# Kernel tuning notes

Measured on AMD Instinct MI355X. Metric: run time of the kernel, lower is better.

Reference implementation:

```python
import jax, jax.numpy as jnp
import numpy as np

# dims
T, B, D = 128, 512, 512          # seq, batch, d_input = dim_aug_state*n_agent
M, H, DH, DFF = 6, 2, 32, 64     # mem_len, heads, d_head_inner, d_ff_inner
ACT = 64                          # dim_action*n_agent
BG = 0.1                          # GRU-gate bias (GTrXL)


def _ln(t, g, b):
    mu = t.mean(-1, keepdims=True)
    var = ((t - mu) ** 2).mean(-1, keepdims=True)
    return (t - mu) / jnp.sqrt(var + 1e-5) * g + b


def _rel_shift(x):
    # x: [T, J, B, H] -> TransformerXL relative shift
    Tq, J = x.shape[0], x.shape[1]
    zp = jnp.zeros((Tq, 1) + x.shape[2:], x.dtype)
    x = jnp.concatenate([zp, x], axis=1)              # [T, J+1, B, H]
    x = x.reshape((J + 1, Tq) + x.shape[2:])[1:]      # [J, T, B, H]
    return x.reshape((Tq, J) + x.shape[2:])


def _gate(x, y, W, b):
    # GRU-style gating g(x, y): x = residual stream, y = new branch output
    lin = lambda t, i: t @ W[i] + b[i]
    r = jax.nn.sigmoid(lin(y, 0) + lin(x, 1))
    z = jax.nn.sigmoid(lin(y, 2) + lin(x, 3) - BG)
    h = jnp.tanh(lin(y, 4) + (r * x) @ W[5] + b[5])
    return (1.0 - z) * x + z * h


def setup_inputs() -> dict:
    key = jax.random.key(0)
    ks = iter(jax.random.split(key, 32))
    rn = lambda shape, s=0.02: jax.random.normal(next(ks), shape, jnp.float32) * s
    return dict(
        aug_states=jax.random.normal(next(ks), (T, B, D), jnp.float32),
        action=jax.random.normal(next(ks), (B, ACT), jnp.float32),
        memory=jnp.zeros((M, B, D), jnp.float32),
        W_q=rn((D, H * DH)), W_kv=rn((D, 2 * H * DH)), W_p=rn((D, H * DH)), W_out=rn((H * DH, D)),
        u=rn((H, DH)), v=rn((H, DH)),
        ln1_g=jnp.ones(D), ln1_b=jnp.zeros(D), ln2_g=jnp.ones(D), ln2_b=jnp.zeros(D),
        ff_W1=rn((D, DFF)), ff_b1=jnp.zeros(DFF), ff_W2=rn((DFF, D)), ff_b2=jnp.zeros(D),
        g1_W=rn((6, D, D)), g1_b=jnp.zeros((6, D)), g2_W=rn((6, D, D)), g2_b=jnp.zeros((6, D)),
        d1_W=rn((D, 1024)), d1_b=jnp.zeros(1024),
        d2_W=rn((1024 + ACT, 512)), d2_b=jnp.zeros(512),
        d3_W=rn((512, 300)), d3_b=jnp.zeros(300),
        d4_W=rn((300, 1)), d4_b=jnp.zeros(1),
    )


def reference(aug_states, action, memory, W_q, W_kv, W_p, W_out, u, v,
              ln1_g, ln1_b, ln2_g, ln2_b, ff_W1, ff_b1, ff_W2, ff_b2,
              g1_W, g1_b, g2_W, g2_b, d1_W, d1_b, d2_W, d2_b, d3_W, d3_b, d4_W, d4_b):
    x = aug_states                                    # [T, B, D]
    J = T + M
    # sinusoidal relative position embeddings for positions J-1 .. 0
    pos = jnp.arange(J - 1, -1, -1.0, dtype=jnp.float32)
    inv_freq = 1.0 / (10000.0 ** (jnp.arange(0, D, 2, dtype=jnp.float32) / D))
    si = pos[:, None] * inv_freq[None, :]
    pos_emb = jnp.concatenate([jnp.sin(si), jnp.cos(si)], axis=-1)   # [J, D]

    # --- stable (pre-LN + gated) TransformerXL layer ---
    src2 = _ln(x, ln1_g, ln1_b)
    cat = jnp.concatenate([memory, src2], axis=0)     # [J, B, D]
    k, vv = jnp.split(cat @ W_kv, 2, axis=-1)
    q = (src2 @ W_q).reshape(T, B, H, DH)
    k = k.reshape(J, B, H, DH)
    vv = vv.reshape(J, B, H, DH)
    p = (pos_emb @ W_p).reshape(J, H, DH)
    content = jnp.einsum("ibhd,jbhd->ijbh", q + u, k)
    position = _rel_shift(jnp.einsum("ibhd,jhd->ijbh", q + v, p))
    attn = content + position                         # [T, J, B, H]
    mask = jnp.arange(J)[None, :] > (jnp.arange(T)[:, None] + M)     # causal w/ memory offset
    attn = jnp.where(mask[:, :, None, None], -jnp.inf, attn)
    attn = jax.nn.softmax(attn * (1.0 / np.sqrt(DH)), axis=1)
    av = jnp.einsum("ijbh,jbhd->ibhd", attn, vv).reshape(T, B, H * DH)
    src = _gate(x, av @ W_out, g1_W, g1_b)
    ff = jax.nn.relu(_ln(src, ln2_g, ln2_b) @ ff_W1 + ff_b1) @ ff_W2 + ff_b2
    out = _gate(src, ff, g2_W, g2_b)                  # [T, B, D]

    # --- mean pool + MLP critic head ---
    ts = out.mean(axis=0)                             # [B, D]
    h1 = jax.nn.relu(ts @ d1_W + d1_b)
    h = jnp.concatenate([h1, action], axis=1)
    h = jax.nn.relu(h @ d2_W + d2_b)
    h = jax.nn.relu(h @ d3_W + d3_b)
    return jax.nn.relu(h @ d4_W + d4_b)               # [B, 1]
```

## Files before the change

### kernel.cpp

```cpp
#include <hip/hip_runtime.h>
#include <math.h>

namespace {

constexpr int kT = 128, kB = 512, kD = 512, kM = 6, kH = 2;
constexpr int kJ = kT + kM;
constexpr float kBG = 0.1f;
constexpr int kTB = kT * kB;
constexpr int kBK = 32;

typedef __attribute__((ext_vector_type(8))) short bf16x8;
typedef __attribute__((ext_vector_type(4))) float f32x4;
typedef __attribute__((ext_vector_type(8))) unsigned short us8;
typedef __attribute__((ext_vector_type(4))) unsigned short us4;

__device__ __forceinline__ float sigmoidf_(float x) {
  return 1.0f / (1.0f + __expf(-x));
}

__device__ __forceinline__ unsigned short bf16u(float f) {
  union { float f; unsigned u; } c; c.f = f;
  unsigned r = c.u + 0x7fffu + ((c.u >> 16) & 1u);
  return (unsigned short)(r >> 16);
}

__device__ __forceinline__ float b2f(unsigned short u) {
  union { unsigned u; float f; } c; c.u = (unsigned)u << 16;
  return c.f;
}

__device__ __forceinline__ void gl_lds16(const void* g, void* l) {
  __builtin_amdgcn_global_load_lds(
      (const __attribute__((address_space(1))) unsigned int*)g,
      (__attribute__((address_space(3))) unsigned int*)l, 16, 0, 0);
}

__global__ __launch_bounds__(256) void transp_kernel(const float* __restrict__ W,
                                                     unsigned short* __restrict__ Wt,
                                                     int K, int N) {
  __shared__ float t[32][33];
  const int n0 = blockIdx.x * 32, k0 = blockIdx.y * 32;
  const float* Wb = W + (size_t)blockIdx.z * K * N;
  unsigned short* Wtb = Wt + (size_t)blockIdx.z * K * N;
  int tx = threadIdx.x & 31, ty = threadIdx.x >> 5;
#pragma unroll
  for (int r = 0; r < 32; r += 8)
    t[ty + r][tx] = Wb[(size_t)(k0 + ty + r) * N + n0 + tx];
  __syncthreads();
#pragma unroll
  for (int r = 0; r < 32; r += 8)
    Wtb[(size_t)(n0 + ty + r) * K + k0 + tx] = bf16u(t[tx][ty + r]);
}

__global__ __launch_bounds__(256) void conv_bf16_kernel(const float* __restrict__ in,
                                                        unsigned short* __restrict__ outb,
                                                        size_t n) {
  size_t idx = ((size_t)blockIdx.x * 256 + threadIdx.x) * 8;
  if (idx >= n) return;
  float4 a = *(const float4*)(in + idx);
  float4 c = *(const float4*)(in + idx + 4);
  us8 o;
  o[0] = bf16u(a.x); o[1] = bf16u(a.y); o[2] = bf16u(a.z); o[3] = bf16u(a.w);
  o[4] = bf16u(c.x); o[5] = bf16u(c.y); o[6] = bf16u(c.z); o[7] = bf16u(c.w);
  *(us8*)(outb + idx) = o;
}

__global__ __launch_bounds__(256) void ln1_dual_kernel(const float* __restrict__ in,
                                                       const float* __restrict__ g,
                                                       const float* __restrict__ b,
                                                       unsigned short* __restrict__ outLN,
                                                       unsigned short* __restrict__ outRaw,
                                                       int nrows) {
  int wave = threadIdx.x >> 6, lane = threadIdx.x & 63;
  int row = blockIdx.x * 4 + wave;
  if (row >= nrows) return;
  const float* p = in + (size_t)row * kD + lane * 8;
  float4 a = *(const float4*)p;
  float4 c = *(const float4*)(p + 4);
  float v[8] = {a.x, a.y, a.z, a.w, c.x, c.y, c.z, c.w};
  float s = 0.f;
#pragma unroll
  for (int i = 0; i < 8; ++i) s += v[i];
#pragma unroll
  for (int off = 32; off; off >>= 1) s += __shfl_xor(s, off);
  float mu = s * (1.0f / 512.0f);
  float q = 0.f;
#pragma unroll
  for (int i = 0; i < 8; ++i) { float d = v[i] - mu; q += d * d; }
#pragma unroll
  for (int off = 32; off; off >>= 1) q += __shfl_xor(q, off);
  float rstd = rsqrtf(q * (1.0f / 512.0f) + 1e-5f);
  us8 oln, oraw;
#pragma unroll
  for (int i = 0; i < 8; ++i) {
    int col = lane * 8 + i;
    oln[i] = bf16u((v[i] - mu) * rstd * g[col] + b[col]);
    oraw[i] = bf16u(v[i]);
  }
  size_t off8 = (size_t)row * kD + lane * 8;
  *(us8*)(outLN + off8) = oln;
  *(us8*)(outRaw + off8) = oraw;
}

__global__ __launch_bounds__(256) void ln_b16_kernel(const unsigned short* __restrict__ in,
                                                     const float* __restrict__ g,
                                                     const float* __restrict__ b,
                                                     unsigned short* __restrict__ outb,
                                                     int nrows) {
  int wave = threadIdx.x >> 6, lane = threadIdx.x & 63;
  int row = blockIdx.x * 4 + wave;
  if (row >= nrows) return;
  us8 iv = *(const us8*)(in + (size_t)row * kD + lane * 8);
  float v[8];
#pragma unroll
  for (int i = 0; i < 8; ++i) v[i] = b2f(iv[i]);
  float s = 0.f;
#pragma unroll
  for (int i = 0; i < 8; ++i) s += v[i];
#pragma unroll
  for (int off = 32; off; off >>= 1) s += __shfl_xor(s, off);
  float mu = s * (1.0f / 512.0f);
  float q = 0.f;
#pragma unroll
  for (int i = 0; i < 8; ++i) { float d = v[i] - mu; q += d * d; }
#pragma unroll
  for (int off = 32; off; off >>= 1) q += __shfl_xor(q, off);
  float rstd = rsqrtf(q * (1.0f / 512.0f) + 1e-5f);
  us8 o;
#pragma unroll
  for (int i = 0; i < 8; ++i) {
    int col = lane * 8 + i;
    o[i] = bf16u((v[i] - mu) * rstd * g[col] + b[col]);
  }
  *(us8*)(outb + (size_t)row * kD + lane * 8) = o;
}

template <int TN, int EPI>
__global__ __launch_bounds__(256) void mfma_gemm_bt(
    const unsigned short* __restrict__ A, const unsigned short* __restrict__ Bt,
    int K, const float* __restrict__ bias, void* __restrict__ Cv, int N) {
  constexpr int MI = (TN == 128) ? 4 : 2;
  constexpr int NJ = 4;
  constexpr int BCH = TN * 64 / 1024;
  __shared__ __align__(16) unsigned short As[2][128 * kBK];
  __shared__ __align__(16) unsigned short Bs[2][TN * kBK];
  const int tid = threadIdx.x;
  const int lane = tid & 63, wv = tid >> 6;
  const int ml = lane & 15, qd = lane >> 4;
  const int m0 = blockIdx.y * 128, n0 = blockIdx.x * TN;
  const int mw0 = (TN == 128) ? (wv >> 1) * 64 : wv * 32;
  const int nw0 = (TN == 128) ? (wv & 1) * 64 : 0;
  const size_t ldA = (size_t)K * 2, ldB = (size_t)K * 2;
  const char* Ab = (const char*)A + (size_t)m0 * ldA;
  const char* Bb = (const char*)Bt + (size_t)n0 * ldB;
  auto stg = [&](int k0, int buf) {
#pragma unroll
    for (int c = wv; c < 8; c += 4) {
      int fb = c * 1024 + lane * 16;
      gl_lds16(Ab + (size_t)(fb >> 6) * ldA + (fb & 63) + (size_t)k0 * 2,
               (char*)As[buf] + c * 1024);
    }
#pragma unroll
    for (int c = wv; c < BCH; c += 4) {
      int fb = c * 1024 + lane * 16;
      gl_lds16(Bb + (size_t)(fb >> 6) * ldB + (fb & 63) + (size_t)k0 * 2,
               (char*)Bs[buf] + c * 1024);
    }
  };
  f32x4 acc[MI][NJ];
#pragma unroll
  for (int i = 0; i < MI; ++i)
#pragma unroll
    for (int j = 0; j < NJ; ++j) acc[i][j] = (f32x4)0.f;
  stg(0, 0);
  __syncthreads();
  int cur = 0;
  for (int k0 = 0; k0 < K; k0 += kBK) {
    if (k0 + kBK < K) stg(k0 + kBK, cur ^ 1);
    bf16x8 af[MI], bfr[NJ];
#pragma unroll
    for (int i = 0; i < MI; ++i)
      af[i] = *(const bf16x8*)(As[cur] + (mw0 + i * 16 + ml) * kBK + qd * 8);
#pragma unroll
    for (int j = 0; j < NJ; ++j)
      bfr[j] = *(const bf16x8*)(Bs[cur] + (nw0 + j * 16 + ml) * kBK + qd * 8);
#pragma unroll
    for (int i = 0; i < MI; ++i)
#pragma unroll
      for (int j = 0; j < NJ; ++j)
        acc[i][j] = __builtin_amdgcn_mfma_f32_16x16x32_bf16(af[i], bfr[j], acc[i][j], 0, 0, 0);
    __syncthreads();
    cur ^= 1;
  }
#pragma unroll
  for (int i = 0; i < MI; ++i)
#pragma unroll
    for (int j = 0; j < NJ; ++j)
#pragma unroll
      for (int r = 0; r < 4; ++r) {
        int m = m0 + mw0 + i * 16 + qd * 4 + r;
        int n = n0 + nw0 + j * 16 + ml;
        float val = acc[i][j][r];
        if (EPI >= 2) val += bias[n];
        if (EPI == 2) val = fmaxf(val, 0.f);
        size_t idx = (size_t)m * N + n;
        if (EPI == 0) ((float*)Cv)[idx] = val;
        else ((unsigned short*)Cv)[idx] = bf16u(val);
      }
}

template <int NBLOG>
__device__ __forceinline__ void xcd_decode(int& m0, int& n0, int tileN) {
  const int L = blockIdx.x;
  const int xcd = L & 7;
  const int s = L >> 3;
  const int mgPerX = (int)(gridDim.x >> (3 + NBLOG));
  const int mg = xcd * mgPerX + (s >> NBLOG);
  const int nb = s & ((1 << NBLOG) - 1);
  m0 = mg * 128;
  n0 = nb * tileN;
}

__global__ __launch_bounds__(512, 4) void mfma_gate_r(
    const unsigned short* __restrict__ Yb, const unsigned short* __restrict__ Xb,
    const unsigned short* __restrict__ Wt, const float* __restrict__ gb,
    unsigned short* __restrict__ RX) {
  __shared__ __align__(16) unsigned short As[2][128 * kBK];
  __shared__ __align__(16) unsigned short Bs[2][256 * kBK];
  const int tid = threadIdx.x;
  const int lane = tid & 63, wv = tid >> 6;
  const int ml = lane & 15, qd = lane >> 4;
  int m0, n0;
  xcd_decode<1>(m0, n0, 256);
  const int mw0 = (wv & 1) * 64, nw0 = (wv >> 1) * 64;
  const size_t ld = (size_t)kD * 2;
  const size_t DD = (size_t)kD * kD;
  const char* Abp[2], *Bbp[2];
  {
    const unsigned short* Ap[2] = {Yb, Xb};
#pragma unroll
    for (int p = 0; p < 2; ++p) {
      Abp[p] = (const char*)Ap[p] + (size_t)m0 * ld;
      Bbp[p] = (const char*)(Wt + (size_t)p * DD) + (size_t)n0 * ld;
    }
  }
  auto stg = [&](const char* Ab, const char* Bb, int k0, int buf) {
    {
      int fb = wv * 1024 + lane * 16;
      gl_lds16(Ab + (size_t)(fb >> 6) * ld + (fb & 63) + (size_t)k0 * 2,
               (char*)As[buf] + wv * 1024);
    }
#pragma unroll
    for (int c = wv; c < 16; c += 8) {
      int fb = c * 1024 + lane * 16;
      gl_lds16(Bb + (size_t)(fb >> 6) * ld + (fb & 63) + (size_t)k0 * 2,
               (char*)Bs[buf] + c * 1024);
    }
  };
  f32x4 acc[4][4];
#pragma unroll
  for (int i = 0; i < 4; ++i)
#pragma unroll
    for (int j = 0; j < 4; ++j) acc[i][j] = (f32x4)0.f;
  stg(Abp[0], Bbp[0], 0, 0);
  __syncthreads();
  int cur = 0;
#pragma unroll
  for (int p = 0; p < 2; ++p) {
    for (int k = 0; k < 16; ++k) {
      if (k < 15) stg(Abp[p], Bbp[p], (k + 1) * kBK, cur ^ 1);
      else if (p < 1) stg(Abp[p + 1], Bbp[p + 1], 0, cur ^ 1);
      bf16x8 af[4], bfr[4];
#pragma unroll
      for (int i = 0; i < 4; ++i)
        af[i] = *(const bf16x8*)(As[cur] + (mw0 + i * 16 + ml) * kBK + qd * 8);
#pragma unroll
      for (int j = 0; j < 4; ++j)
        bfr[j] = *(const bf16x8*)(Bs[cur] + (nw0 + j * 16 + ml) * kBK + qd * 8);
#pragma unroll
      for (int i = 0; i < 4; ++i)
#pragma unroll
        for (int j = 0; j < 4; ++j)
          acc[i][j] = __builtin_amdgcn_mfma_f32_16x16x32_bf16(af[i], bfr[j], acc[i][j], 0, 0, 0);
      __syncthreads();
      cur ^= 1;
    }
  }
#pragma unroll
  for (int i = 0; i < 4; ++i)
#pragma unroll
    for (int j = 0; j < 4; ++j)
#pragma unroll
      for (int r = 0; r < 4; ++r) {
        int m = m0 + mw0 + i * 16 + qd * 4 + r;
        int n = n0 + nw0 + j * 16 + ml;
        float rg = sigmoidf_(acc[i][j][r] + gb[n] + gb[kD + n]);
        size_t idx = (size_t)m * kD + n;
        RX[idx] = bf16u(rg * b2f(Xb[idx]));
      }
}

template <bool POOL>
__global__ __launch_bounds__(512, 4) void mfma_gate_hz(
    const unsigned short* __restrict__ Yb, const unsigned short* __restrict__ RXb,
    const unsigned short* __restrict__ Xb, const unsigned short* __restrict__ Wt,
    const float* __restrict__ gb, unsigned short* __restrict__ OUTb,
    float* __restrict__ TS, int rowoff) {
  __shared__ __align__(16) unsigned short As[2][128 * kBK];
  __shared__ __align__(16) unsigned short Bs[2][128 * kBK];
  const int tid = threadIdx.x;
  const int lane = tid & 63, wv = tid >> 6;
  const int ml = lane & 15, qd = lane >> 4;
  int m0, n0;
  xcd_decode<2>(m0, n0, 128);
  const int mw0 = (wv & 3) * 32, nw0 = (wv >> 2) * 64;
  const size_t ld = (size_t)kD * 2;
  const size_t DD = (size_t)kD * kD;
  f32x4 accH[2][4], accZ[2][4];
#pragma unroll
  for (int i = 0; i < 2; ++i)
#pragma unroll
    for (int j = 0; j < 4; ++j) { accH[i][j] = (f32x4)0.f; accZ[i][j] = (f32x4)0.f; }
  const char* Abp[4], *Bbp[4];
  {
    const unsigned short* Ap[4] = {Yb, RXb, Yb, Xb};
    const int wsel[4] = {4, 5, 2, 3};
#pragma unroll
    for (int p = 0; p < 4; ++p) {
      Abp[p] = (const char*)Ap[p] + (size_t)m0 * ld;
      Bbp[p] = (const char*)(Wt + (size_t)wsel[p] * DD) + (size_t)n0 * ld;
    }
  }
  auto stg = [&](const char* Ab, const char* Bb, int k0, int buf) {
    int fb = wv * 1024 + lane * 16;
    size_t go = (size_t)(fb >> 6) * ld + (fb & 63) + (size_t)k0 * 2;
    gl_lds16(Ab + go, (char*)As[buf] + wv * 1024);
    gl_lds16(Bb + go, (char*)Bs[buf] + wv * 1024);
  };
  stg(Abp[0], Bbp[0], 0, 0);
  __syncthreads();
  int cur = 0;
#pragma unroll
  for (int p = 0; p < 4; ++p) {
    f32x4 (*acc)[4] = (p < 2) ? accH : accZ;
    for (int k = 0; k < 16; ++k) {
      if (k < 15) stg(Abp[p], Bbp[p], (k + 1) * kBK, cur ^ 1);
      else if (p < 3) stg(Abp[p + 1], Bbp[p + 1], 0, cur ^ 1);
      bf16x8 af[2], bfr[4];
#pragma unroll
      for (int i = 0; i < 2; ++i)
        af[i] = *(const bf16x8*)(As[cur] + (mw0 + i * 16 + ml) * kBK + qd * 8);
#pragma unroll
      for (int j = 0; j < 4; ++j)
        bfr[j] = *(const bf16x8*)(Bs[cur] + (nw0 + j * 16 + ml) * kBK + qd * 8);
#pragma unroll
      for (int i = 0; i < 2; ++i)
#pragma unroll
        for (int j = 0; j < 4; ++j)
          acc[i][j] = __builtin_amdgcn_mfma_f32_16x16x32_bf16(af[i], bfr[j], acc[i][j], 0, 0, 0);
      __syncthreads();
      cur ^= 1;
    }
  }
#pragma unroll
  for (int i = 0; i < 2; ++i)
#pragma unroll
    for (int j = 0; j < 4; ++j)
#pragma unroll
      for (int r = 0; r < 4; ++r) {
        int m = m0 + mw0 + i * 16 + qd * 4 + r;
        int n = n0 + nw0 + j * 16 + ml;
        float z = sigmoidf_(accZ[i][j][r] + gb[2 * kD + n] + gb[3 * kD + n] - kBG);
        float hc = tanhf(accH[i][j][r] + gb[4 * kD + n] + gb[5 * kD + n]);
        size_t idx = (size_t)m * kD + n;
        float val = (1.0f - z) * b2f(Xb[idx]) + z * hc;
        if (POOL) {
          int b = (rowoff + m) & (kB - 1);
          atomicAdd(TS + (size_t)b * kD + n, val * (1.0f / kT));
        } else {
          OUTb[idx] = bf16u(val);
        }
      }
}

__global__ __launch_bounds__(64) void posp_kernel(const float* __restrict__ Wp,
                                                  float* __restrict__ P) {
  __shared__ float emb[512];
  int jj = blockIdx.x;
  int t = threadIdx.x;
  float pos = (float)(kJ - 1 - jj);
#pragma unroll
  for (int r = 0; r < 8; ++r) {
    int d = t + r * 64;
    int i = (d < 256) ? d : d - 256;
    float invf = expf(-((float)(2 * i) * (1.0f / 512.0f)) * 9.210340371976184f);
    float si = pos * invf;
    emb[d] = (d < 256) ? sinf(si) : cosf(si);
  }
  __syncthreads();
  float acc = 0.f;
  for (int d = 0; d < 512; ++d) acc = fmaf(emb[d], Wp[d * 64 + t], acc);
  P[jj * 64 + t] = acc;
}

__global__ __launch_bounds__(128) void attn_kernel(
    const float* __restrict__ Q, const unsigned short* __restrict__ KV,
    const float* __restrict__ P, const float* __restrict__ U,
    const float* __restrict__ V, unsigned short* __restrict__ AV) {
  __shared__ float ks[kJ][32];
  __shared__ float vs[kJ][32];
  __shared__ float ps[32][kJ + 2];
  const int b = blockIdx.x, h = blockIdx.y;
  const int tid = threadIdx.x;
  for (int idx = tid; idx < kJ * 8; idx += 128) {
    int j = idx >> 3, seg = idx & 7;
    const unsigned short* src = KV + ((size_t)(j * kB + b)) * 128 + h * 32 + seg * 4;
    us4 kq = *(const us4*)src;
    us4 vq = *(const us4*)(src + 64);
#pragma unroll
    for (int e = 0; e < 4; ++e) {
      ks[j][seg * 4 + e] = b2f(kq[e]);
      vs[j][seg * 4 + e] = b2f(vq[e]);
    }
  }
  for (int idx = tid; idx < kJ * 8; idx += 128) {
    int j = idx >> 3, seg = idx & 7;
    float4 pq = *(const float4*)(P + j * 64 + h * 32 + seg * 4);
    ps[seg * 4 + 0][j] = pq.x;
    ps[seg * 4 + 1][j] = pq.y;
    ps[seg * 4 + 2][j] = pq.z;
    ps[seg * 4 + 3][j] = pq.w;
  }
  __syncthreads();
  const int i = tid;
  float qu[32], qv[32];
  const float* qp = Q + ((size_t)(i * kB + b)) * 64 + h * 32;
#pragma unroll
  for (int d = 0; d < 32; ++d) {
    float qd = qp[d];
    qu[d] = qd + U[h * 32 + d];
    qv[d] = qd + V[h * 32 + d];
  }
  float m = -INFINITY, l = 0.f, acc[32] = {};
  const float scale = 0.17677669529663687f;
  for (int j = 0; j <= i + kM; ++j) {
    float s = 0.f;
#pragma unroll
    for (int d = 0; d < 32; d += 4) {
      float4 k4 = *(const float4*)&ks[j][d];
      s = fmaf(qu[d + 0], k4.x, s);
      s = fmaf(qu[d + 1], k4.y, s);
      s = fmaf(qu[d + 2], k4.z, s);
      s = fmaf(qu[d + 3], k4.w, s);
    }
    int jj = j + (kT - 1) - i;
#pragma unroll
    for (int d = 0; d < 32; ++d) s = fmaf(qv[d], ps[d][jj], s);
    float ls = s * scale;
    float nm = fmaxf(m, ls);
    float w = __expf(ls - nm);
    float f = __expf(m - nm);
    l = l * f + w;
#pragma unroll
    for (int d = 0; d < 32; d += 4) {
      float4 v4 = *(const float4*)&vs[j][d];
      acc[d + 0] = fmaf(acc[d + 0], f, w * v4.x);
      acc[d + 1] = fmaf(acc[d + 1], f, w * v4.y);
      acc[d + 2] = fmaf(acc[d + 2], f, w * v4.z);
      acc[d + 3] = fmaf(acc[d + 3], f, w * v4.w);
    }
    m = nm;
  }
  float inv = 1.0f / l;
  unsigned short* o = AV + ((size_t)(i * kB + b)) * 64 + h * 32;
#pragma unroll
  for (int d = 0; d < 32; ++d) o[d] = bf16u(acc[d] * inv);
}

template <int ACTF, bool DUAL>
__global__ __launch_bounds__(256) void gemm_kernel(
    const float* __restrict__ A1, const float* __restrict__ Bm1, int K1,
    const float* __restrict__ A2, const float* __restrict__ Bm2, int K2,
    const float* __restrict__ bias, float* __restrict__ C, int Mrows, int N) {
  __shared__ float As[16][68];
  __shared__ float Bs[16][68];
  const int tid = threadIdx.x;
  const int tx = tid & 15, ty = tid >> 4;
  const int m0 = blockIdx.y * 64, n0 = blockIdx.x * 64;
  const int ar = tid >> 2, aseg = tid & 3;
  float acc[4][4] = {};
#pragma unroll
  for (int pass = 0; pass < (DUAL ? 2 : 1); ++pass) {
    const float* A = (DUAL && pass) ? A2 : A1;
    const float* Bm = (DUAL && pass) ? Bm2 : Bm1;
    const int K = (DUAL && pass) ? K2 : K1;
    for (int k0 = 0; k0 < K; k0 += 16) {
      {
        int row = m0 + ar;
        int kb = k0 + aseg * 4;
        float x0 = 0.f, x1 = 0.f, x2 = 0.f, x3 = 0.f;
        if (row < Mrows) {
          const float* ap = A + (size_t)row * K + kb;
          if (kb + 3 < K) {
            float4 t = *(const float4*)ap;
            x0 = t.x; x1 = t.y; x2 = t.z; x3 = t.w;
          } else {
            if (kb + 0 < K) x0 = ap[0];
            if (kb + 1 < K) x1 = ap[1];
            if (kb + 2 < K) x2 = ap[2];
          }
        }
        As[aseg * 4 + 0][ar] = x0;
        As[aseg * 4 + 1][ar] = x1;
        As[aseg * 4 + 2][ar] = x2;
        As[aseg * 4 + 3][ar] = x3;
      }
      {
        int krow = k0 + ty;
        int nb = n0 + tx * 4;
        float y0 = 0.f, y1 = 0.f, y2 = 0.f, y3 = 0.f;
        if (krow < K) {
          const float* bp = Bm + (size_t)krow * N + nb;
          if (nb + 3 < N) {
            float4 t = *(const float4*)bp;
            y0 = t.x; y1 = t.y; y2 = t.z; y3 = t.w;
          } else {
            if (nb + 0 < N) y0 = bp[0];
            if (nb + 1 < N) y1 = bp[1];
            if (nb + 2 < N) y2 = bp[2];
          }
        }
        *(float4*)&Bs[ty][tx * 4] = make_float4(y0, y1, y2, y3);
      }
      __syncthreads();
#pragma unroll
      for (int kk = 0; kk < 16; ++kk) {
        float a[4], bb[4];
        *(float4*)a = *(const float4*)&As[kk][ty * 4];
        *(float4*)bb = *(const float4*)&Bs[kk][tx * 4];
#pragma unroll
        for (int i = 0; i < 4; ++i)
#pragma unroll
          for (int j = 0; j < 4; ++j) acc[i][j] = fmaf(a[i], bb[j], acc[i][j]);
      }
      __syncthreads();
    }
  }
#pragma unroll
  for (int i = 0; i < 4; ++i) {
    int m = m0 + ty * 4 + i;
    if (m >= Mrows) continue;
#pragma unroll
    for (int j = 0; j < 4; ++j) {
      int n = n0 + tx * 4 + j;
      if (n >= N) continue;
      float val = acc[i][j];
      if (bias) val += bias[n];
      if (ACTF == 1) val = fmaxf(val, 0.f);
      C[(size_t)m * N + n] = val;
    }
  }
}

}

extern "C" void kernel_launch(void* const* d_in, const int* in_sizes, int n_in,
                              void* d_out, int out_size, void* d_ws, size_t ws_size,
                              hipStream_t stream) {
  (void)in_sizes; (void)n_in; (void)out_size;
  const float* aug    = (const float*)d_in[0];
  const float* action = (const float*)d_in[1];
  const float* memory = (const float*)d_in[2];
  const float* W_q    = (const float*)d_in[3];
  const float* W_kv   = (const float*)d_in[4];
  const float* W_p    = (const float*)d_in[5];
  const float* W_out  = (const float*)d_in[6];
  const float* u      = (const float*)d_in[7];
  const float* v      = (const float*)d_in[8];
  const float* ln1_g  = (const float*)d_in[9];
  const float* ln1_b  = (const float*)d_in[10];
  const float* ln2_g  = (const float*)d_in[11];
  const float* ln2_b  = (const float*)d_in[12];
  const float* ff_W1  = (const float*)d_in[13];
  const float* ff_b1  = (const float*)d_in[14];
  const float* ff_W2  = (const float*)d_in[15];
  const float* ff_b2  = (const float*)d_in[16];
  const float* g1_W   = (const float*)d_in[17];
  const float* g1_b   = (const float*)d_in[18];
  const float* g2_W   = (const float*)d_in[19];
  const float* g2_b   = (const float*)d_in[20];
  const float* d1_W   = (const float*)d_in[21];
  const float* d1_b   = (const float*)d_in[22];
  const float* d2_W   = (const float*)d_in[23];
  const float* d2_b   = (const float*)d_in[24];
  const float* d3_W   = (const float*)d_in[25];
  const float* d3_b   = (const float*)d_in[26];
  const float* d4_W   = (const float*)d_in[27];
  const float* d4_b   = (const float*)d_in[28];
  float* out = (float*)d_out;

  char* base = (char*)d_ws;
  auto alloc = [&](size_t bytes) -> char* {
    char* p = base;
    base += (bytes + 255) & ~(size_t)255;
    return p;
  };
  unsigned short* Wqt  = (unsigned short*)alloc((size_t)64 * 512 * 2);
  unsigned short* Wkvt = (unsigned short*)alloc((size_t)128 * 512 * 2);
  unsigned short* Wot  = (unsigned short*)alloc((size_t)512 * 64 * 2);
  unsigned short* Wf1t = (unsigned short*)alloc((size_t)64 * 512 * 2);
  unsigned short* Wf2t = (unsigned short*)alloc((size_t)512 * 64 * 2);
  unsigned short* G1t  = (unsigned short*)alloc((size_t)6 * 512 * 512 * 2);
  unsigned short* G2t  = (unsigned short*)alloc((size_t)6 * 512 * 512 * 2);
  unsigned short* Memb = (unsigned short*)alloc((size_t)3072 * 512 * 2);
  unsigned short* KVb  = (unsigned short*)alloc((size_t)kJ * kB * 128 * 2);
  float* Qb  = (float*)alloc((size_t)kTB * 64 * 4);
  unsigned short* AVb = (unsigned short*)alloc((size_t)kTB * 64 * 2);
  unsigned short* Xb  = (unsigned short*)alloc((size_t)kTB * kD * 2);
  float* Pb  = (float*)alloc((size_t)kJ * 64 * 4);
  float* TSb = (float*)alloc((size_t)kB * kD * 4);
  float* H1b = (float*)alloc((size_t)kB * 1024 * 4);
  float* H2b = (float*)alloc((size_t)kB * 512 * 4);
  float* H3b = (float*)alloc((size_t)kB * 320 * 4);
  size_t fixedBytes = (size_t)(base - (char*)d_ws);
  const size_t ln1Bytes = (size_t)kTB * kD * 2;
  int nch = 1;
  while (nch < 32) {
    size_t chunkBytes = (size_t)(kTB / nch) * 4224 + 4096;
    size_t reuse = chunkBytes > ln1Bytes ? chunkBytes : ln1Bytes;
    if (fixedBytes + reuse <= ws_size) break;
    nch <<= 1;
  }
  const int CR = kTB / nch;
  char* R = base;
  unsigned short* L1b = (unsigned short*)R;
  char* rp = R;
  auto ralloc = [&](size_t bytes) -> char* {
    char* p = rp;
    rp += (bytes + 255) & ~(size_t)255;
    return p;
  };
  unsigned short* Ycb   = (unsigned short*)ralloc((size_t)CR * 512 * 2);
  unsigned short* RXcb  = (unsigned short*)ralloc((size_t)CR * 512 * 2);
  unsigned short* SRCcb = (unsigned short*)ralloc((size_t)CR * 512 * 2);
  unsigned short* LN2cb = (unsigned short*)ralloc((size_t)CR * 512 * 2);
  unsigned short* F1cb  = (unsigned short*)ralloc((size_t)CR * 64 * 2);

  const float* np = nullptr;
  const int MG = CR / 128;

  hipMemsetAsync(TSb, 0, (size_t)kB * kD * sizeof(float), stream);
  transp_kernel<<<dim3(2, 16, 1), 256, 0, stream>>>(W_q, Wqt, 512, 64);
  transp_kernel<<<dim3(4, 16, 1), 256, 0, stream>>>(W_kv, Wkvt, 512, 128);
  transp_kernel<<<dim3(16, 2, 1), 256, 0, stream>>>(W_out, Wot, 64, 512);
  transp_kernel<<<dim3(2, 16, 1), 256, 0, stream>>>(ff_W1, Wf1t, 512, 64);
  transp_kernel<<<dim3(16, 2, 1), 256, 0, stream>>>(ff_W2, Wf2t, 64, 512);
  transp_kernel<<<dim3(16, 16, 6), 256, 0, stream>>>(g1_W, G1t, 512, 512);
  transp_kernel<<<dim3(16, 16, 6), 256, 0, stream>>>(g2_W, G2t, 512, 512);
  conv_bf16_kernel<<<(3072 * 512 / 8 + 255) / 256, 256, 0, stream>>>(
      memory, Memb, (size_t)3072 * 512);
  ln1_dual_kernel<<<kTB / 4, 256, 0, stream>>>(aug, ln1_g, ln1_b, L1b, Xb, kTB);
  mfma_gemm_bt<128, 1><<<dim3(1, 3072 / 128), 256, 0, stream>>>(
      Memb, Wkvt, 512, np, KVb, 128);
  mfma_gemm_bt<128, 1><<<dim3(1, kTB / 128), 256, 0, stream>>>(
      L1b, Wkvt, 512, np, KVb + (size_t)3072 * 128, 128);
  mfma_gemm_bt<64, 0><<<dim3(1, kTB / 128), 256, 0, stream>>>(
      L1b, Wqt, 512, np, Qb, 64);
  posp_kernel<<<kJ, 64, 0, stream>>>(W_p, Pb);
  attn_kernel<<<dim3(kB, kH), 128, 0, stream>>>(Qb, KVb, Pb, u, v, AVb);

  for (int c = 0; c < nch; ++c) {
    const int R0 = c * CR;
    const unsigned short* Xc = Xb + (size_t)R0 * kD;
    mfma_gemm_bt<128, 1><<<dim3(4, MG), 256, 0, stream>>>(
        AVb + (size_t)R0 * 64, Wot, 64, np, Ycb, 512);
    mfma_gate_r<<<2 * MG, 512, 0, stream>>>(Ycb, Xc, G1t, g1_b, RXcb);
    mfma_gate_hz<false><<<4 * MG, 512, 0, stream>>>(
        Ycb, RXcb, Xc, G1t, g1_b, SRCcb, nullptr, R0);
    ln_b16_kernel<<<CR / 4, 256, 0, stream>>>(SRCcb, ln2_g, ln2_b, LN2cb, CR);
    mfma_gemm_bt<64, 2><<<dim3(1, MG), 256, 0, stream>>>(
        LN2cb, Wf1t, 512, ff_b1, F1cb, 64);
    mfma_gemm_bt<128, 3><<<dim3(4, MG), 256, 0, stream>>>(
        F1cb, Wf2t, 64, ff_b2, Ycb, 512);
    mfma_gate_r<<<2 * MG, 512, 0, stream>>>(Ycb, SRCcb, G2t, g2_b, RXcb);
    mfma_gate_hz<true><<<4 * MG, 512, 0, stream>>>(
        Ycb, RXcb, SRCcb, G2t, g2_b, nullptr, TSb, R0);
  }

  gemm_kernel<1, false><<<dim3(16, kB / 64), 256, 0, stream>>>(
      TSb, d1_W, 512, np, np, 0, d1_b, H1b, kB, 1024);
  gemm_kernel<1, true><<<dim3(8, kB / 64), 256, 0, stream>>>(
      H1b, d2_W, 1024, action, d2_W + (size_t)1024 * 512, 64, d2_b, H2b, kB, 512);
  gemm_kernel<1, false><<<dim3(5, kB / 64), 256, 0, stream>>>(
      H2b, d3_W, 512, np, np, 0, d3_b, H3b, kB, 300);
  gemm_kernel<1, false><<<dim3(1, kB / 64), 256, 0, stream>>>(
      H3b, d4_W, 300, np, np, 0, d4_b, out, kB, 1);
}
```

Baseline: 1.550 ms.

## Triple-buffer LDS staging with explicit vmcnt waits in MFMA GEMM kernels

```diff
diff --git a/kernel.cpp b/kernel.cpp
--- a/kernel.cpp
+++ b/kernel.cpp
@@ -34,6 +34,13 @@
       (const __attribute__((address_space(1))) unsigned int*)g,
       (__attribute__((address_space(3))) unsigned int*)l, 16, 0, 0);
 }
+
+template <int N>
+__device__ __forceinline__ void wvm_() {
+  asm volatile("s_waitcnt vmcnt(%0)" :: "n"(N) : "memory");
+}
+__device__ __forceinline__ void bar_() { __builtin_amdgcn_s_barrier(); }
+__device__ __forceinline__ void cfence_() { asm volatile("" ::: "memory"); }
 
 __global__ __launch_bounds__(256) void transp_kernel(const float* __restrict__ W,
                                                      unsigned short* __restrict__ Wt,
@@ -142,8 +149,9 @@
   constexpr int MI = (TN == 128) ? 4 : 2;
   constexpr int NJ = 4;
   constexpr int BCH = TN * 64 / 1024;
-  __shared__ __align__(16) unsigned short As[2][128 * kBK];
-  __shared__ __align__(16) unsigned short Bs[2][TN * kBK];
+  constexpr int NLD = 2 + BCH / 4;
+  __shared__ __align__(16) unsigned short As[3][128 * kBK];
+  __shared__ __align__(16) unsigned short Bs[3][TN * kBK];
   const int tid = threadIdx.x;
   const int lane = tid & 63, wv = tid >> 6;
   const int ml = lane & 15, qd = lane >> 4;
@@ -173,24 +181,28 @@
 #pragma unroll
     for (int j = 0; j < NJ; ++j) acc[i][j] = (f32x4)0.f;
   stg(0, 0);
-  __syncthreads();
-  int cur = 0;
+  stg(kBK, 1);
+  int cb = 0;
   for (int k0 = 0; k0 < K; k0 += kBK) {
-    if (k0 + kBK < K) stg(k0 + kBK, cur ^ 1);
+    const int sb = (cb == 0) ? 2 : cb - 1;
+    if (k0 + 2 * kBK < K) { stg(k0 + 2 * kBK, sb); wvm_<2 * NLD>(); }
+    else if (k0 + kBK < K) { wvm_<NLD>(); }
+    else { wvm_<0>(); }
+    bar_(); cfence_();
     bf16x8 af[MI], bfr[NJ];
 #pragma unroll
     for (int i = 0; i < MI; ++i)
-      af[i] = *(const bf16x8*)(As[cur] + (mw0 + i * 16 + ml) * kBK + qd * 8);
+      af[i] = *(const bf16x8*)(As[cb] + (mw0 + i * 16 + ml) * kBK + qd * 8);
 #pragma unroll
     for (int j = 0; j < NJ; ++j)
-      bfr[j] = *(const bf16x8*)(Bs[cur] + (nw0 + j * 16 + ml) * kBK + qd * 8);
+      bfr[j] = *(const bf16x8*)(Bs[cb] + (nw0 + j * 16 + ml) * kBK + qd * 8);
 #pragma unroll
     for (int i = 0; i < MI; ++i)
 #pragma unroll
       for (int j = 0; j < NJ; ++j)
         acc[i][j] = __builtin_amdgcn_mfma_f32_16x16x32_bf16(af[i], bfr[j], acc[i][j], 0, 0, 0);
-    __syncthreads();
-    cur ^= 1;
+    cfence_(); bar_();
+    cb = (cb == 2) ? 0 : cb + 1;
   }
 #pragma unroll
   for (int i = 0; i < MI; ++i)
@@ -225,8 +237,8 @@
     const unsigned short* __restrict__ Yb, const unsigned short* __restrict__ Xb,
     const unsigned short* __restrict__ Wt, const float* __restrict__ gb,
     unsigned short* __restrict__ RX) {
-  __shared__ __align__(16) unsigned short As[2][128 * kBK];
-  __shared__ __align__(16) unsigned short Bs[2][256 * kBK];
+  __shared__ __align__(16) unsigned short As[3][128 * kBK];
+  __shared__ __align__(16) unsigned short Bs[3][256 * kBK];
   const int tid = threadIdx.x;
   const int lane = tid & 63, wv = tid >> 6;
   const int ml = lane & 15, qd = lane >> 4;
@@ -263,27 +275,31 @@
 #pragma unroll
     for (int j = 0; j < 4; ++j) acc[i][j] = (f32x4)0.f;
   stg(Abp[0], Bbp[0], 0, 0);
-  __syncthreads();
-  int cur = 0;
+  stg(Abp[0], Bbp[0], kBK, 1);
+  int cb = 0;
 #pragma unroll
   for (int p = 0; p < 2; ++p) {
     for (int k = 0; k < 16; ++k) {
-      if (k < 15) stg(Abp[p], Bbp[p], (k + 1) * kBK, cur ^ 1);
-      else if (p < 1) stg(Abp[p + 1], Bbp[p + 1], 0, cur ^ 1);
+      const int sb = (cb == 0) ? 2 : cb - 1;
+      if (k < 14) { stg(Abp[p], Bbp[p], (k + 2) * kBK, sb); wvm_<6>(); }
+      else if (p < 1) { stg(Abp[p + 1], Bbp[p + 1], (k - 14) * kBK, sb); wvm_<6>(); }
+      else if (k == 14) { wvm_<3>(); }
+      else { wvm_<0>(); }
+      bar_(); cfence_();
       bf16x8 af[4], bfr[4];
 #pragma unroll
       for (int i = 0; i < 4; ++i)
-        af[i] = *(const bf16x8*)(As[cur] + (mw0 + i * 16 + ml) * kBK + qd * 8);
+        af[i] = *(const bf16x8*)(As[cb] + (mw0 + i * 16 + ml) * kBK + qd * 8);
 #pragma unroll
       for (int j = 0; j < 4; ++j)
-        bfr[j] = *(const bf16x8*)(Bs[cur] + (nw0 + j * 16 + ml) * kBK + qd * 8);
+        bfr[j] = *(const bf16x8*)(Bs[cb] + (nw0 + j * 16 + ml) * kBK + qd * 8);
 #pragma unroll
       for (int i = 0; i < 4; ++i)
 #pragma unroll
         for (int j = 0; j < 4; ++j)
           acc[i][j] = __builtin_amdgcn_mfma_f32_16x16x32_bf16(af[i], bfr[j], acc[i][j], 0, 0, 0);
-      __syncthreads();
-      cur ^= 1;
+      cfence_(); bar_();
+      cb = (cb == 2) ? 0 : cb + 1;
     }
   }
 #pragma unroll
@@ -306,8 +322,8 @@
     const unsigned short* __restrict__ Xb, const unsigned short* __restrict__ Wt,
     const float* __restrict__ gb, unsigned short* __restrict__ OUTb,
     float* __restrict__ TS, int rowoff) {
-  __shared__ __align__(16) unsigned short As[2][128 * kBK];
-  __shared__ __align__(16) unsigned short Bs[2][128 * kBK];
+  __shared__ __align__(16) unsigned short As[3][128 * kBK];
+  __shared__ __align__(16) unsigned short Bs[3][128 * kBK];
   const int tid = threadIdx.x;
   const int lane = tid & 63, wv = tid >> 6;
   const int ml = lane & 15, qd = lane >> 4;
@@ -338,28 +354,32 @@
     gl_lds16(Bb + go, (char*)Bs[buf] + wv * 1024);
   };
   stg(Abp[0], Bbp[0], 0, 0);
-  __syncthreads();
-  int cur = 0;
+  stg(Abp[0], Bbp[0], kBK, 1);
+  int cb = 0;
 #pragma unroll
   for (int p = 0; p < 4; ++p) {
     f32x4 (*acc)[4] = (p < 2) ? accH : accZ;
     for (int k = 0; k < 16; ++k) {
-      if (k < 15) stg(Abp[p], Bbp[p], (k + 1) * kBK, cur ^ 1);
-      else if (p < 3) stg(Abp[p + 1], Bbp[p + 1], 0, cur ^ 1);
+      const int sb = (cb == 0) ? 2 : cb - 1;
+      if (k < 14) { stg(Abp[p], Bbp[p], (k + 2) * kBK, sb); wvm_<4>(); }
+      else if (p < 3) { stg(Abp[p + 1], Bbp[p + 1], (k - 14) * kBK, sb); wvm_<4>(); }
+      else if (k == 14) { wvm_<2>(); }
+      else { wvm_<0>(); }
+      bar_(); cfence_();
       bf16x8 af[2], bfr[4];
 #pragma unroll
       for (int i = 0; i < 2; ++i)
-        af[i] = *(const bf16x8*)(As[cur] + (mw0 + i * 16 + ml) * kBK + qd * 8);
+        af[i] = *(const bf16x8*)(As[cb] + (mw0 + i * 16 + ml) * kBK + qd * 8);
 #pragma unroll
       for (int j = 0; j < 4; ++j)
-        bfr[j] = *(const bf16x8*)(Bs[cur] + (nw0 + j * 16 + ml) * kBK + qd * 8);
+        bfr[j] = *(const bf16x8*)(Bs[cb] + (nw0 + j * 16 + ml) * kBK + qd * 8);
 #pragma unroll
       for (int i = 0; i < 2; ++i)
 #pragma unroll
         for (int j = 0; j < 4; ++j)
           acc[i][j] = __builtin_amdgcn_mfma_f32_16x16x32_bf16(af[i], bfr[j], acc[i][j], 0, 0, 0);
-      __syncthreads();
-      cur ^= 1;
+      cfence_(); bar_();
+      cb = (cb == 2) ? 0 : cb + 1;
     }
   }
 #pragma unroll
```

New measurement: 1.428 ms. 1.09x faster.
